# Kernel optimization log

Measured on AMD Instinct MI355X. Metric: run time of the kernel, lower is better.

Reference implementation:

```python
import jax, jax.numpy as jnp
import numpy as np
import math

B, S, D = 1, 2048, 2048
NQ, NKV = 32, 8
HD = D // NQ            # 64
NREP = NQ // NKV        # 4
EPS = 1e-6


def _rope_tables(seq_len, head_dim, theta=10000.0):
    half = head_dim // 2
    inv_freq = 1.0 / (theta ** (np.arange(0, half, dtype=np.float32) / half))
    t = np.arange(seq_len, dtype=np.float32)
    freqs = np.outer(t, inv_freq)  # [S, half]
    return jnp.asarray(np.cos(freqs)), jnp.asarray(np.sin(freqs))


def _rmsnorm(x, g, eps=EPS):
    denom = jnp.sqrt(jnp.mean(x * x, axis=-1, keepdims=True) + eps)
    return x / denom * g


def _rope(x, cos, sin):
    # x: [B, S, H, HD]; cos/sin: [S, HD//2]
    half = x.shape[-1] // 2
    x1, x2 = x[..., :half], x[..., half:]
    c = cos[None, :, None, :]
    s = sin[None, :, None, :]
    return jnp.concatenate([x1 * c - x2 * s, x1 * s + x2 * c], axis=-1)


def setup_inputs() -> dict:
    key = jax.random.key(0)
    ks = jax.random.split(key, 6)
    scale = 1.0 / math.sqrt(D)
    x = jax.random.normal(ks[0], (B, S, D), dtype=jnp.float32)
    Wq = jax.random.normal(ks[1], (D, NQ * HD), dtype=jnp.float32) * scale
    Wk = jax.random.normal(ks[2], (D, NKV * HD), dtype=jnp.float32) * scale
    Wv = jax.random.normal(ks[3], (D, NKV * HD), dtype=jnp.float32) * scale
    Wo = jax.random.normal(ks[4], (NQ * HD, D), dtype=jnp.float32) * scale
    g_q = jnp.ones((HD,), dtype=jnp.float32)
    g_k = jnp.ones((HD,), dtype=jnp.float32)
    cos, sin = _rope_tables(S, HD)
    return {"x": x, "cos": cos, "sin": sin, "g_q": g_q, "g_k": g_k,
            "Wq": Wq, "Wk": Wk, "Wv": Wv, "Wo": Wo}


def reference(x, cos, sin, g_q, g_k, Wq, Wk, Wv, Wo):
    bs, seq, _ = x.shape
    Q = (x @ Wq).reshape(bs, seq, NQ, HD)
    K = (x @ Wk).reshape(bs, seq, NKV, HD)
    V = (x @ Wv).reshape(bs, seq, NKV, HD)
    Q = _rope(_rmsnorm(Q, g_q), cos, sin)
    K = _rope(_rmsnorm(K, g_k), cos, sin)
    # GQA: repeat_interleave KV heads to match Q heads
    K = jnp.repeat(K, NREP, axis=2)  # [B,S,NQ,HD]
    V = jnp.repeat(V, NREP, axis=2)
    # scores: [B, H, S, S]
    scores = jnp.einsum('bshd,bthd->bhst', Q, K) / math.sqrt(HD)
    mask = jnp.triu(jnp.ones((seq, seq), dtype=bool), k=1)
    scores = jnp.where(mask, -jnp.inf, scores)
    attn = jax.nn.softmax(scores, axis=-1)
    out = jnp.einsum('bhst,bthd->bshd', attn, V).reshape(bs, seq, NQ * HD)
    return out @ Wo
```

## Files before the change

### kernel.cpp

```cpp
#include <hip/hip_runtime.h>
#include <hip/hip_bf16.h>
#include <math.h>

#define S 2048
#define D 2048
#define NQ 32
#define NKV 8
#define HD 64
#define HALF 32
#define NREP 4
#define QKV_N 3072
#define KCOL 2048
#define VCOL 2560

typedef unsigned short ushort_t;
typedef __attribute__((ext_vector_type(8))) short bf16x8;
typedef __attribute__((ext_vector_type(4))) float f32x4;
typedef float f4 __attribute__((ext_vector_type(4)));

__device__ __forceinline__ ushort_t f2bf(float f) {
    __hip_bfloat16 h = __float2bfloat16(f);
    return *reinterpret_cast<ushort_t*>(&h);
}
__device__ __forceinline__ float bf2f(ushort_t u) {
    __hip_bfloat16 h = *reinterpret_cast<__hip_bfloat16*>(&u);
    return __bfloat162float(h);
}

__device__ __forceinline__ void load_lds16(const ushort_t* g, ushort_t* l) {
    __builtin_amdgcn_global_load_lds(
        (const __attribute__((address_space(1))) unsigned int*)g,
        (__attribute__((address_space(3))) unsigned int*)l,
        16, 0, 0);
}

__global__ __launch_bounds__(256) void prep_all(const float* __restrict__ x,
                                                ushort_t* __restrict__ Xb,
                                                const float* __restrict__ Wq,
                                                const float* __restrict__ Wk,
                                                const float* __restrict__ Wv,
                                                ushort_t* __restrict__ WqkvT) {
    __shared__ float tile[32][33];
    const int b = blockIdx.x;
    if (b < 4096) {
        int i = (b * 256 + threadIdx.x) * 4;
        f4 v = *(const f4*)&x[i];
        Xb[i + 0] = f2bf(v[0]);
        Xb[i + 1] = f2bf(v[1]);
        Xb[i + 2] = f2bf(v[2]);
        Xb[i + 3] = f2bf(v[3]);
        return;
    }
    const float* src; int N, row_off, t;
    if (b < 8192)      { src = Wq; N = 2048; row_off = 0;    t = b - 4096; }
    else if (b < 9216) { src = Wk; N = 512;  row_off = 2048; t = b - 8192; }
    else               { src = Wv; N = 512;  row_off = 2560; t = b - 9216; }
    const int ntn = N / 32;
    const int n0 = (t % ntn) * 32, k0 = (t / ntn) * 32;
    const int tx = threadIdx.x & 31, ty = threadIdx.x >> 5;
    #pragma unroll
    for (int i = 0; i < 32; i += 8)
        tile[ty + i][tx] = src[(size_t)(k0 + ty + i) * N + (n0 + tx)];
    __syncthreads();
    #pragma unroll
    for (int i = 0; i < 32; i += 8)
        WqkvT[(size_t)(row_off + n0 + ty + i) * 2048 + (k0 + tx)] = f2bf(tile[tx][ty + i]);
}

template <typename OutT>
__global__ __launch_bounds__(256) void gemm64(const ushort_t* __restrict__ A,
                                              const ushort_t* __restrict__ BT,
                                              OutT* __restrict__ C,
                                              int M, int N, int Kdim) {
    __shared__ ushort_t As[64][64];
    __shared__ ushort_t Bs[64][64];
    const int tid = threadIdx.x;
    const int w = tid >> 6, lane = tid & 63;
    const int r16 = lane & 15, quad = lane >> 4;
    const int wm = (w >> 1) * 32, wn = (w & 1) * 32;
    const int bm = blockIdx.y * 64, bn = blockIdx.x * 64;
    const int srow = lane >> 3;
    const int jl = (lane & 7) ^ srow;
    const int rx = r16 & 7;

    f32x4 acc[2][2];
    #pragma unroll
    for (int r = 0; r < 2; ++r)
        #pragma unroll
        for (int c = 0; c < 2; ++c) acc[r][c] = (f32x4){0.f, 0.f, 0.f, 0.f};

    for (int k0 = 0; k0 < Kdim; k0 += 64) {
        __syncthreads();
        #pragma unroll
        for (int i = 0; i < 2; ++i) {
            int rbase = w * 16 + i * 8;
            load_lds16(A  + (size_t)(bm + rbase + srow) * Kdim + k0 + jl * 8, &As[rbase][0]);
            load_lds16(BT + (size_t)(bn + rbase + srow) * Kdim + k0 + jl * 8, &Bs[rbase][0]);
        }
        __syncthreads();

        #pragma unroll
        for (int h = 0; h < 2; ++h) {
            bf16x8 af[2], bfr[2];
            #pragma unroll
            for (int r = 0; r < 2; ++r)
                af[r]  = *(const bf16x8*)&As[wm + 16 * r + r16][((quad + 4 * h) ^ rx) * 8];
            #pragma unroll
            for (int c = 0; c < 2; ++c)
                bfr[c] = *(const bf16x8*)&Bs[wn + 16 * c + r16][((quad + 4 * h) ^ rx) * 8];
            #pragma unroll
            for (int r = 0; r < 2; ++r)
                #pragma unroll
                for (int c = 0; c < 2; ++c)
                    acc[r][c] = __builtin_amdgcn_mfma_f32_16x16x32_bf16(af[r], bfr[c], acc[r][c], 0, 0, 0);
        }
    }

    #pragma unroll
    for (int r = 0; r < 2; ++r)
        #pragma unroll
        for (int c = 0; c < 2; ++c)
            #pragma unroll
            for (int reg = 0; reg < 4; ++reg) {
                int row = bm + wm + 16 * r + quad * 4 + reg;
                int col = bn + wn + 16 * c + r16;
                float v = acc[r][c][reg];
                if constexpr (sizeof(OutT) == 2) C[(size_t)row * N + col] = (OutT)f2bf(v);
                else                             C[(size_t)row * N + col] = (OutT)v;
            }
}

__global__ __launch_bounds__(256) void rms_rope_vwo(ushort_t* __restrict__ QKV,
                                                    const float* __restrict__ gq,
                                                    const float* __restrict__ gk,
                                                    const float* __restrict__ cosT,
                                                    const float* __restrict__ sinT,
                                                    ushort_t* __restrict__ VTg,
                                                    const float* __restrict__ Wo,
                                                    ushort_t* __restrict__ WoT) {
    const int y = blockIdx.y, xb = blockIdx.x;
    if (y < 10) {
        const int s = xb;
        const int w = threadIdx.x >> 6;
        const int hh = y * 4 + w;
        const int d = threadIdx.x & 63;
        const float* g;
        int col;
        if (hh < NQ) { g = gq; col = hh * HD; }
        else         { g = gk; col = KCOL + (hh - NQ) * HD; }
        ushort_t* xp = QKV + (size_t)s * QKV_N + col;
        float v = bf2f(xp[d]);
        float ss = v * v;
        #pragma unroll
        for (int off = 32; off > 0; off >>= 1) ss += __shfl_down(ss, off);
        ss = __shfl(ss, 0);
        float inv = rsqrtf(ss * (1.0f / HD) + 1e-6f);
        float xn = v * inv * g[d];
        float other = __shfl(xn, d ^ 32);
        float c = cosT[(size_t)s * HALF + (d & 31)];
        float sn = sinT[(size_t)s * HALF + (d & 31)];
        float outv = (d < HALF) ? (xn * c - other * sn) : (other * sn + xn * c);
        xp[d] = f2bf(outv);
        return;
    }
    const int tx = threadIdx.x & 31, ty = threadIdx.x >> 5;
    if (y == 10 && xb < 1024) {
        __shared__ ushort_t vt[32][33];
        const int s0 = (xb & 63) * 32, d0 = (xb >> 6) * 32;
        #pragma unroll
        for (int i = 0; i < 32; i += 8)
            vt[ty + i][tx] = QKV[(size_t)(s0 + ty + i) * QKV_N + VCOL + d0 + tx];
        __syncthreads();
        #pragma unroll
        for (int i = 0; i < 32; i += 8)
            VTg[(size_t)(d0 + ty + i) * S + s0 + tx] = vt[tx][ty + i];
        return;
    }
    int idx;
    if (y == 10)      idx = xb - 1024;
    else if (y == 11) idx = 1024 + xb;
    else              idx = 3072 + xb;
    if (idx < 0 || idx >= 4096) return;
    __shared__ float wt[32][33];
    const int n0 = (idx & 63) * 32, k0 = (idx >> 6) * 32;
    #pragma unroll
    for (int i = 0; i < 32; i += 8)
        wt[ty + i][tx] = Wo[(size_t)(k0 + ty + i) * 2048 + (n0 + tx)];
    __syncthreads();
    #pragma unroll
    for (int i = 0; i < 32; i += 8)
        WoT[(size_t)(n0 + ty + i) * 2048 + (k0 + tx)] = f2bf(wt[tx][ty + i]);
}

__global__ __launch_bounds__(256) void zero_acc(f4* __restrict__ AccBuf4,
                                                f4* __restrict__ AccL4) {
    int i = blockIdx.x * 256 + threadIdx.x;
    if (i < 524288) AccBuf4[i] = (f4){0.f, 0.f, 0.f, 0.f};
    else if (i < 532480) AccL4[i - 524288] = (f4){0.f, 0.f, 0.f, 0.f};
}

__global__ __launch_bounds__(256) void flash_attn_mfma(const ushort_t* __restrict__ QKV,
                                                       const ushort_t* __restrict__ VTg,
                                                       ushort_t* __restrict__ O,
                                                       float* __restrict__ AccBuf,
                                                       float* __restrict__ AccL) {
    __shared__ ushort_t Ks[2][32][64];
    __shared__ ushort_t Vt[2][64][32];
    __shared__ ushort_t Ps[4][16][40];

    const int bx = blockIdx.x;
    int qt, tb, te;
    bool atom;
    if (bx < 16) { qt = 16 + bx; tb = 0; te = 32; atom = true; }
    else         { qt = 47 - bx; atom = (qt >= 16); tb = atom ? 32 : 0; te = 2 * qt + 2; }

    const int q0 = qt * 64;
    const int h  = blockIdx.y;
    const int kvh = h >> 2;
    const int tid = threadIdx.x;
    const int w = tid >> 6, lane = tid & 63;
    const int r16 = lane & 15, quad = lane >> 4;
    const int kcol = KCOL + kvh * HD;
    const int vtrow0 = kvh * HD;
    const int krow = lane >> 3;
    const int jl = (lane & 7) ^ krow;
    const int vrow = lane >> 2;
    const int jv = (lane & 3) ^ (vrow & 3);
    const int rx = r16 & 7;
    const int rx3 = r16 & 3;

    const ushort_t* qrow = QKV + (size_t)(q0 + 16 * w + r16) * QKV_N + h * HD;
    bf16x8 qf0, qf1;
    {
        bf16x8 r0 = *(const bf16x8*)(qrow + quad * 8);
        bf16x8 r1 = *(const bf16x8*)(qrow + quad * 8 + 32);
        #pragma unroll
        for (int j = 0; j < 8; ++j) {
            qf0[j] = (short)f2bf(bf2f((ushort_t)r0[j]) * 0.18033688f);
            qf1[j] = (short)f2bf(bf2f((ushort_t)r1[j]) * 0.18033688f);
        }
    }

    bf16x8 onesf;
    {
        ushort_t ov = (r16 == 0) ? (ushort_t)0x3F80 : (ushort_t)0;
        #pragma unroll
        for (int j = 0; j < 8; ++j) onesf[j] = (short)ov;
    }

    f32x4 accO[4];
    f32x4 accL = (f32x4){0.f, 0.f, 0.f, 0.f};
    #pragma unroll
    for (int c = 0; c < 4; ++c) accO[c] = (f32x4){0.f, 0.f, 0.f, 0.f};

    auto stage = [&](int b, int t) {
        const int kb = t * 32;
        load_lds16(QKV + (size_t)(kb + w * 8 + krow) * QKV_N + kcol + jl * 8,
                   &Ks[b][w * 8][0]);
        load_lds16(VTg + (size_t)(vtrow0 + w * 16 + vrow) * S + kb + jv * 8,
                   &Vt[b][w * 16][0]);
    };

    stage(tb & 1, tb);

    for (int t = tb; t < te; ++t) {
        __syncthreads();
        if (t + 1 < te) stage((t + 1) & 1, t + 1);

        const ushort_t (*K_)[64] = Ks[t & 1];
        const ushort_t (*V_)[32] = Vt[t & 1];
        const int rel = t * 32 - q0;
        const bool maskt = (rel >= 0);

        f32x4 sc[2];
        #pragma unroll
        for (int c = 0; c < 2; ++c) {
            bf16x8 kf0 = *(const bf16x8*)&K_[16 * c + r16][(quad ^ rx) * 8];
            bf16x8 kf1 = *(const bf16x8*)&K_[16 * c + r16][((quad + 4) ^ rx) * 8];
            f32x4 z = (f32x4){0.f, 0.f, 0.f, 0.f};
            z = __builtin_amdgcn_mfma_f32_16x16x32_bf16(qf0, kf0, z, 0, 0, 0);
            z = __builtin_amdgcn_mfma_f32_16x16x32_bf16(qf1, kf1, z, 0, 0, 0);
            sc[c] = z;
        }

        #pragma unroll
        for (int c = 0; c < 2; ++c)
            #pragma unroll
            for (int reg = 0; reg < 4; ++reg) {
                float v = sc[c][reg];
                if (maskt && (rel + 16 * c + r16 > 16 * w + quad * 4 + reg)) v = -INFINITY;
                Ps[w][quad * 4 + reg][16 * c + r16] = f2bf(exp2f(v));
            }

        bf16x8 pf = *(const bf16x8*)&Ps[w][r16][quad * 8];

        accL = __builtin_amdgcn_mfma_f32_16x16x32_bf16(pf, onesf, accL, 0, 0, 0);
        #pragma unroll
        for (int c = 0; c < 4; ++c) {
            bf16x8 vf = *(const bf16x8*)&V_[16 * c + r16][(quad ^ rx3) * 8];
            accO[c] = __builtin_amdgcn_mfma_f32_16x16x32_bf16(pf, vf, accO[c], 0, 0, 0);
        }
    }

    if (!atom) {
        #pragma unroll
        for (int reg = 0; reg < 4; ++reg) {
            float l = __shfl(accL[reg], lane & 48);
            float invl = 1.0f / l;
            int row = q0 + 16 * w + quad * 4 + reg;
            ushort_t* op = O + (size_t)row * D + h * HD;
            #pragma unroll
            for (int c = 0; c < 4; ++c)
                op[16 * c + r16] = f2bf(accO[c][reg] * invl);
        }
    } else {
        const int pair = (qt - 16) * 32 + h;
        float* ab = AccBuf + (size_t)pair * 4096;
        #pragma unroll
        for (int reg = 0; reg < 4; ++reg) {
            int row = 16 * w + quad * 4 + reg;
            #pragma unroll
            for (int c = 0; c < 4; ++c)
                atomicAdd(&ab[row * 64 + 16 * c + r16], accO[c][reg]);
        }
        if (r16 == 0) {
            #pragma unroll
            for (int reg = 0; reg < 4; ++reg)
                atomicAdd(&AccL[pair * 64 + 16 * w + quad * 4 + reg], accL[reg]);
        }
    }
}

__global__ __launch_bounds__(256) void normalize_o(const float* __restrict__ AccBuf,
                                                   const float* __restrict__ AccL,
                                                   ushort_t* __restrict__ O) {
    const int pair = blockIdx.x;
    const int qt = 16 + (pair >> 5);
    const int h  = pair & 31;
    const float* ab = AccBuf + (size_t)pair * 4096;
    const float* lp = AccL + pair * 64;
    for (int i = threadIdx.x; i < 4096; i += 256) {
        int row = i >> 6, d = i & 63;
        O[(size_t)(qt * 64 + row) * D + h * HD + d] = f2bf(ab[i] / lp[row]);
    }
}

extern "C" void kernel_launch(void* const* d_in, const int* in_sizes, int n_in,
                              void* d_out, int out_size, void* d_ws, size_t ws_size,
                              hipStream_t stream) {
    const float* x    = (const float*)d_in[0];
    const float* cosT = (const float*)d_in[1];
    const float* sinT = (const float*)d_in[2];
    const float* g_q  = (const float*)d_in[3];
    const float* g_k  = (const float*)d_in[4];
    const float* Wq   = (const float*)d_in[5];
    const float* Wk   = (const float*)d_in[6];
    const float* Wv   = (const float*)d_in[7];
    const float* Wo   = (const float*)d_in[8];
    float* out = (float*)d_out;

    char* base = (char*)d_ws;
    ushort_t* Xb    = (ushort_t*)base;
    ushort_t* WqkvT = (ushort_t*)(base + 8388608);
    ushort_t* QKVb  = (ushort_t*)(base + 20971520);
    ushort_t* WoT   = (ushort_t*)(base + 8388608);
    ushort_t* VTg   = (ushort_t*)(base + 16777216);
    float*    AccL  = (float*)(base + 18874368);
    float*    AccBuf = (float*)d_out;
    ushort_t* Ob    = Xb;

    prep_all<<<10240, 256, 0, stream>>>(x, Xb, Wq, Wk, Wv, WqkvT);
    gemm64<ushort_t><<<dim3(QKV_N / 64, S / 64), 256, 0, stream>>>(Xb, WqkvT, QKVb, S, QKV_N, D);
    rms_rope_vwo<<<dim3(2048, 13), 256, 0, stream>>>(QKVb, g_q, g_k, cosT, sinT, VTg, Wo, WoT);
    zero_acc<<<2080, 256, 0, stream>>>((f4*)AccBuf, (f4*)AccL);
    flash_attn_mfma<<<dim3(48, NQ), 256, 0, stream>>>(QKVb, VTg, Ob, AccBuf, AccL);
    normalize_o<<<512, 256, 0, stream>>>(AccBuf, AccL, Ob);
    gemm64<float><<<dim3(D / 64, S / 64), 256, 0, stream>>>(Ob, WoT, out, S, D, D);
}
```

Before: 257.5 us.

## Fuse RMSNorm/RoPE and V transpose into QKV GEMM epilogue, widen attention KV tiles

Adds a dedicated QKV GEMM whose epilogue applies RMSNorm and RoPE per head and writes V already transposed, which removes the separate rms_rope_vwo pass and its extra read and write of QKV. The accumulator zeroing moves into prep_all and the Wo transpose moves into the normalize kernel, cutting two launches. Flash attention now processes 64-key tiles instead of 32, halving loop iterations and barriers at the cost of more LDS. Workspace buffers are relocated into the output region.

```diff
diff --git a/kernel.cpp b/kernel.cpp
--- a/kernel.cpp
+++ b/kernel.cpp
@@ -16,6 +16,7 @@
 typedef unsigned short ushort_t;
 typedef __attribute__((ext_vector_type(8))) short bf16x8;
 typedef __attribute__((ext_vector_type(4))) float f32x4;
+typedef __attribute__((ext_vector_type(4))) unsigned short us4;
 typedef float f4 __attribute__((ext_vector_type(4)));
 
 __device__ __forceinline__ ushort_t f2bf(float f) {
@@ -39,7 +40,9 @@
                                                 const float* __restrict__ Wq,
                                                 const float* __restrict__ Wk,
                                                 const float* __restrict__ Wv,
-                                                ushort_t* __restrict__ WqkvT) {
+                                                ushort_t* __restrict__ WqkvT,
+                                                f4* __restrict__ AccBuf4,
+                                                f4* __restrict__ AccL4) {
     __shared__ float tile[32][33];
     const int b = blockIdx.x;
     if (b < 4096) {
@@ -51,6 +54,16 @@
         Xb[i + 3] = f2bf(v[3]);
         return;
     }
+    if (b >= 10240) {
+        if (b < 12288) {
+            int i = (b - 10240) * 256 + threadIdx.x;
+            AccBuf4[i] = (f4){0.f, 0.f, 0.f, 0.f};
+        } else {
+            int i = (b - 12288) * 256 + threadIdx.x;
+            if (i < 8192) AccL4[i] = (f4){0.f, 0.f, 0.f, 0.f};
+        }
+        return;
+    }
     const float* src; int N, row_off, t;
     if (b < 8192)      { src = Wq; N = 2048; row_off = 0;    t = b - 4096; }
     else if (b < 9216) { src = Wk; N = 512;  row_off = 2048; t = b - 8192; }
@@ -65,6 +78,117 @@
     #pragma unroll
     for (int i = 0; i < 32; i += 8)
         WqkvT[(size_t)(row_off + n0 + ty + i) * 2048 + (k0 + tx)] = f2bf(tile[tx][ty + i]);
+}
+
+__global__ __launch_bounds__(256) void gemm_qkv(const ushort_t* __restrict__ A,
+                                                const ushort_t* __restrict__ BT,
+                                                ushort_t* __restrict__ QKVb,
+                                                ushort_t* __restrict__ VTg,
+                                                const float* __restrict__ gq,
+                                                const float* __restrict__ gk,
+                                                const float* __restrict__ cosT,
+                                                const float* __restrict__ sinT) {
+    __shared__ ushort_t SM[8448];
+    ushort_t (*As)[32] = (ushort_t(*)[32])SM;
+    ushort_t (*Bs)[32] = (ushort_t(*)[32])(SM + 4096);
+    ushort_t (*Epi)[66] = (ushort_t(*)[66])SM;
+
+    const int tid = threadIdx.x;
+    const int w = tid >> 6, lane = tid & 63;
+    const int r16 = lane & 15, quad = lane >> 4;
+    const int wm = (w >> 1) * 64, wn = (w & 1) * 32;
+    const int bm = blockIdx.y * 128;
+    const int hcol = blockIdx.x;
+    const int bn = hcol * 64;
+    const int sr = lane >> 2;
+    const int sc8 = (lane & 3) * 8;
+
+    f32x4 acc[4][2];
+    #pragma unroll
+    for (int r = 0; r < 4; ++r)
+        #pragma unroll
+        for (int c = 0; c < 2; ++c) acc[r][c] = (f32x4){0.f, 0.f, 0.f, 0.f};
+
+    for (int k0 = 0; k0 < 2048; k0 += 32) {
+        __syncthreads();
+        #pragma unroll
+        for (int i = 0; i < 2; ++i) {
+            int rowt = w * 32 + i * 16;
+            load_lds16(A + (size_t)(bm + rowt + sr) * 2048 + k0 + sc8, &As[rowt][0]);
+        }
+        load_lds16(BT + (size_t)(bn + w * 16 + sr) * 2048 + k0 + sc8, &Bs[w * 16][0]);
+        __syncthreads();
+
+        bf16x8 af[4], bfr[2];
+        #pragma unroll
+        for (int r = 0; r < 4; ++r) af[r]  = *(const bf16x8*)&As[wm + 16 * r + r16][quad * 8];
+        #pragma unroll
+        for (int c = 0; c < 2; ++c) bfr[c] = *(const bf16x8*)&Bs[wn + 16 * c + r16][quad * 8];
+        #pragma unroll
+        for (int r = 0; r < 4; ++r)
+            #pragma unroll
+            for (int c = 0; c < 2; ++c)
+                acc[r][c] = __builtin_amdgcn_mfma_f32_16x16x32_bf16(af[r], bfr[c], acc[r][c], 0, 0, 0);
+    }
+
+    if (hcol >= 40) {
+        const int vd0 = (hcol - 40) * 64;
+        #pragma unroll
+        for (int r = 0; r < 4; ++r)
+            #pragma unroll
+            for (int c = 0; c < 2; ++c) {
+                int col = wn + 16 * c + r16;
+                int row0 = wm + 16 * r + quad * 4;
+                us4 pk;
+                #pragma unroll
+                for (int reg = 0; reg < 4; ++reg) pk[reg] = f2bf(acc[r][c][reg]);
+                *(us4*)&VTg[(size_t)(vd0 + col) * S + bm + row0] = pk;
+            }
+        return;
+    }
+
+    __syncthreads();
+    #pragma unroll
+    for (int r = 0; r < 4; ++r)
+        #pragma unroll
+        for (int c = 0; c < 2; ++c)
+            #pragma unroll
+            for (int reg = 0; reg < 4; ++reg)
+                Epi[wm + 16 * r + quad * 4 + reg][wn + 16 * c + r16] = f2bf(acc[r][c][reg]);
+    __syncthreads();
+
+    const float* g = (hcol < 32) ? gq : gk;
+    const int colbase = (hcol < 32) ? hcol * 64 : KCOL + (hcol - 32) * 64;
+    const int row = tid >> 1;
+    const int half = tid & 1;
+    const int cbase = half * 32;
+    const int s_glob = bm + row;
+
+    float xv[32], pv[32];
+    float ss = 0.f;
+    #pragma unroll
+    for (int j = 0; j < 32; ++j) {
+        xv[j] = bf2f(Epi[row][cbase + j]);
+        pv[j] = bf2f(Epi[row][(cbase ^ 32) + j]);
+        ss += xv[j] * xv[j];
+    }
+    ss += __shfl_xor(ss, 1);
+    float inv = rsqrtf(ss * (1.0f / HD) + 1e-6f);
+
+    ushort_t outp[32];
+    #pragma unroll
+    for (int j = 0; j < 32; ++j) {
+        float xn = xv[j] * inv * g[cbase + j];
+        float xp = pv[j] * inv * g[(cbase ^ 32) + j];
+        float cs = cosT[(size_t)s_glob * HALF + j];
+        float sn = sinT[(size_t)s_glob * HALF + j];
+        float o = half ? (xp * sn + xn * cs) : (xn * cs - xp * sn);
+        outp[j] = f2bf(o);
+    }
+    ushort_t* dst = QKVb + (size_t)s_glob * QKV_N + colbase + cbase;
+    #pragma unroll
+    for (int j = 0; j < 32; j += 8)
+        *(bf16x8*)&dst[j] = *(const bf16x8*)&outp[j];
 }
 
 template <typename OutT>
@@ -130,89 +254,20 @@
             }
 }
 
-__global__ __launch_bounds__(256) void rms_rope_vwo(ushort_t* __restrict__ QKV,
-                                                    const float* __restrict__ gq,
-                                                    const float* __restrict__ gk,
-                                                    const float* __restrict__ cosT,
-                                                    const float* __restrict__ sinT,
-                                                    ushort_t* __restrict__ VTg,
-                                                    const float* __restrict__ Wo,
-                                                    ushort_t* __restrict__ WoT) {
-    const int y = blockIdx.y, xb = blockIdx.x;
-    if (y < 10) {
-        const int s = xb;
-        const int w = threadIdx.x >> 6;
-        const int hh = y * 4 + w;
-        const int d = threadIdx.x & 63;
-        const float* g;
-        int col;
-        if (hh < NQ) { g = gq; col = hh * HD; }
-        else         { g = gk; col = KCOL + (hh - NQ) * HD; }
-        ushort_t* xp = QKV + (size_t)s * QKV_N + col;
-        float v = bf2f(xp[d]);
-        float ss = v * v;
-        #pragma unroll
-        for (int off = 32; off > 0; off >>= 1) ss += __shfl_down(ss, off);
-        ss = __shfl(ss, 0);
-        float inv = rsqrtf(ss * (1.0f / HD) + 1e-6f);
-        float xn = v * inv * g[d];
-        float other = __shfl(xn, d ^ 32);
-        float c = cosT[(size_t)s * HALF + (d & 31)];
-        float sn = sinT[(size_t)s * HALF + (d & 31)];
-        float outv = (d < HALF) ? (xn * c - other * sn) : (other * sn + xn * c);
-        xp[d] = f2bf(outv);
-        return;
-    }
-    const int tx = threadIdx.x & 31, ty = threadIdx.x >> 5;
-    if (y == 10 && xb < 1024) {
-        __shared__ ushort_t vt[32][33];
-        const int s0 = (xb & 63) * 32, d0 = (xb >> 6) * 32;
-        #pragma unroll
-        for (int i = 0; i < 32; i += 8)
-            vt[ty + i][tx] = QKV[(size_t)(s0 + ty + i) * QKV_N + VCOL + d0 + tx];
-        __syncthreads();
-        #pragma unroll
-        for (int i = 0; i < 32; i += 8)
-            VTg[(size_t)(d0 + ty + i) * S + s0 + tx] = vt[tx][ty + i];
-        return;
-    }
-    int idx;
-    if (y == 10)      idx = xb - 1024;
-    else if (y == 11) idx = 1024 + xb;
-    else              idx = 3072 + xb;
-    if (idx < 0 || idx >= 4096) return;
-    __shared__ float wt[32][33];
-    const int n0 = (idx & 63) * 32, k0 = (idx >> 6) * 32;
-    #pragma unroll
-    for (int i = 0; i < 32; i += 8)
-        wt[ty + i][tx] = Wo[(size_t)(k0 + ty + i) * 2048 + (n0 + tx)];
-    __syncthreads();
-    #pragma unroll
-    for (int i = 0; i < 32; i += 8)
-        WoT[(size_t)(n0 + ty + i) * 2048 + (k0 + tx)] = f2bf(wt[tx][ty + i]);
-}
-
-__global__ __launch_bounds__(256) void zero_acc(f4* __restrict__ AccBuf4,
-                                                f4* __restrict__ AccL4) {
-    int i = blockIdx.x * 256 + threadIdx.x;
-    if (i < 524288) AccBuf4[i] = (f4){0.f, 0.f, 0.f, 0.f};
-    else if (i < 532480) AccL4[i - 524288] = (f4){0.f, 0.f, 0.f, 0.f};
-}
-
 __global__ __launch_bounds__(256) void flash_attn_mfma(const ushort_t* __restrict__ QKV,
                                                        const ushort_t* __restrict__ VTg,
                                                        ushort_t* __restrict__ O,
                                                        float* __restrict__ AccBuf,
                                                        float* __restrict__ AccL) {
-    __shared__ ushort_t Ks[2][32][64];
-    __shared__ ushort_t Vt[2][64][32];
-    __shared__ ushort_t Ps[4][16][40];
+    __shared__ ushort_t Ks[2][64][64];
+    __shared__ ushort_t Vt[2][64][64];
+    __shared__ ushort_t Ps[4][16][72];
 
     const int bx = blockIdx.x;
     int qt, tb, te;
     bool atom;
-    if (bx < 16) { qt = 16 + bx; tb = 0; te = 32; atom = true; }
-    else         { qt = 47 - bx; atom = (qt >= 16); tb = atom ? 32 : 0; te = 2 * qt + 2; }
+    if (bx < 16) { qt = 16 + bx; tb = 0; te = 16; atom = true; }
+    else         { qt = 47 - bx; atom = (qt >= 16); tb = atom ? 16 : 0; te = qt + 1; }
 
     const int q0 = qt * 64;
     const int h  = blockIdx.y;
@@ -222,12 +277,9 @@
     const int r16 = lane & 15, quad = lane >> 4;
     const int kcol = KCOL + kvh * HD;
     const int vtrow0 = kvh * HD;
-    const int krow = lane >> 3;
-    const int jl = (lane & 7) ^ krow;
-    const int vrow = lane >> 2;
-    const int jv = (lane & 3) ^ (vrow & 3);
+    const int rsub = lane >> 3;
+    const int jlog = (lane & 7) ^ rsub;
     const int rx = r16 & 7;
-    const int rx3 = r16 & 3;
 
     const ushort_t* qrow = QKV + (size_t)(q0 + 16 * w + r16) * QKV_N + h * HD;
     bf16x8 qf0, qf1;
@@ -253,28 +305,29 @@
     #pragma unroll
     for (int c = 0; c < 4; ++c) accO[c] = (f32x4){0.f, 0.f, 0.f, 0.f};
 
-    auto stage = [&](int b, int t) {
-        const int kb = t * 32;
-        load_lds16(QKV + (size_t)(kb + w * 8 + krow) * QKV_N + kcol + jl * 8,
-                   &Ks[b][w * 8][0]);
-        load_lds16(VTg + (size_t)(vtrow0 + w * 16 + vrow) * S + kb + jv * 8,
-                   &Vt[b][w * 16][0]);
+    auto stage = [&](int b, int t0) {
+        #pragma unroll
+        for (int i = 0; i < 2; ++i) {
+            int base = w * 16 + i * 8;
+            int row = base + rsub;
+            load_lds16(QKV + (size_t)(t0 + row) * QKV_N + kcol + jlog * 8, &Ks[b][base][0]);
+            load_lds16(VTg + (size_t)(vtrow0 + row) * S + t0 + jlog * 8, &Vt[b][base][0]);
+        }
     };
 
-    stage(tb & 1, tb);
+    stage(tb & 1, tb * 64);
 
     for (int t = tb; t < te; ++t) {
         __syncthreads();
-        if (t + 1 < te) stage((t + 1) & 1, t + 1);
+        if (t + 1 < te) stage((t + 1) & 1, (t + 1) * 64);
 
         const ushort_t (*K_)[64] = Ks[t & 1];
-        const ushort_t (*V_)[32] = Vt[t & 1];
-        const int rel = t * 32 - q0;
-        const bool maskt = (rel >= 0);
-
-        f32x4 sc[2];
-        #pragma unroll
-        for (int c = 0; c < 2; ++c) {
+        const ushort_t (*V_)[64] = Vt[t & 1];
+        const bool diag = (t == qt);
+
+        f32x4 sc[4];
+        #pragma unroll
+        for (int c = 0; c < 4; ++c) {
             bf16x8 kf0 = *(const bf16x8*)&K_[16 * c + r16][(quad ^ rx) * 8];
             bf16x8 kf1 = *(const bf16x8*)&K_[16 * c + r16][((quad + 4) ^ rx) * 8];
             f32x4 z = (f32x4){0.f, 0.f, 0.f, 0.f};
@@ -284,21 +337,26 @@
         }
 
         #pragma unroll
-        for (int c = 0; c < 2; ++c)
+        for (int c = 0; c < 4; ++c)
             #pragma unroll
             for (int reg = 0; reg < 4; ++reg) {
                 float v = sc[c][reg];
-                if (maskt && (rel + 16 * c + r16 > 16 * w + quad * 4 + reg)) v = -INFINITY;
+                if (diag && (16 * c + r16 > 16 * w + quad * 4 + reg)) v = -INFINITY;
                 Ps[w][quad * 4 + reg][16 * c + r16] = f2bf(exp2f(v));
             }
 
-        bf16x8 pf = *(const bf16x8*)&Ps[w][r16][quad * 8];
-
-        accL = __builtin_amdgcn_mfma_f32_16x16x32_bf16(pf, onesf, accL, 0, 0, 0);
+        bf16x8 pf0 = *(const bf16x8*)&Ps[w][r16][quad * 8];
+        bf16x8 pf1 = *(const bf16x8*)&Ps[w][r16][quad * 8 + 32];
+
+        accL = __builtin_amdgcn_mfma_f32_16x16x32_bf16(pf0, onesf, accL, 0, 0, 0);
+        accL = __builtin_amdgcn_mfma_f32_16x16x32_bf16(pf1, onesf, accL, 0, 0, 0);
+
         #pragma unroll
         for (int c = 0; c < 4; ++c) {
-            bf16x8 vf = *(const bf16x8*)&V_[16 * c + r16][(quad ^ rx3) * 8];
-            accO[c] = __builtin_amdgcn_mfma_f32_16x16x32_bf16(pf, vf, accO[c], 0, 0, 0);
+            bf16x8 vf0 = *(const bf16x8*)&V_[16 * c + r16][(quad ^ rx) * 8];
+            bf16x8 vf1 = *(const bf16x8*)&V_[16 * c + r16][((quad + 4) ^ rx) * 8];
+            accO[c] = __builtin_amdgcn_mfma_f32_16x16x32_bf16(pf0, vf0, accO[c], 0, 0, 0);
+            accO[c] = __builtin_amdgcn_mfma_f32_16x16x32_bf16(pf1, vf1, accO[c], 0, 0, 0);
         }
     }
 
@@ -331,18 +389,34 @@
     }
 }
 
-__global__ __launch_bounds__(256) void normalize_o(const float* __restrict__ AccBuf,
-                                                   const float* __restrict__ AccL,
-                                                   ushort_t* __restrict__ O) {
-    const int pair = blockIdx.x;
-    const int qt = 16 + (pair >> 5);
-    const int h  = pair & 31;
-    const float* ab = AccBuf + (size_t)pair * 4096;
-    const float* lp = AccL + pair * 64;
-    for (int i = threadIdx.x; i < 4096; i += 256) {
-        int row = i >> 6, d = i & 63;
-        O[(size_t)(qt * 64 + row) * D + h * HD + d] = f2bf(ab[i] / lp[row]);
-    }
+__global__ __launch_bounds__(256) void normalize_wo(const float* __restrict__ AccBuf,
+                                                    const float* __restrict__ AccL,
+                                                    ushort_t* __restrict__ O,
+                                                    const float* __restrict__ Wo,
+                                                    ushort_t* __restrict__ WoT) {
+    const int b = blockIdx.x;
+    if (b < 512) {
+        const int qt = 16 + (b >> 5);
+        const int h  = b & 31;
+        const float* ab = AccBuf + (size_t)b * 4096;
+        const float* lp = AccL + b * 64;
+        for (int i = threadIdx.x; i < 4096; i += 256) {
+            int row = i >> 6, d = i & 63;
+            O[(size_t)(qt * 64 + row) * D + h * HD + d] = f2bf(ab[i] / lp[row]);
+        }
+        return;
+    }
+    __shared__ float wt[32][33];
+    const int idx = b - 512;
+    const int n0 = (idx & 63) * 32, k0 = (idx >> 6) * 32;
+    const int tx = threadIdx.x & 31, ty = threadIdx.x >> 5;
+    #pragma unroll
+    for (int i = 0; i < 32; i += 8)
+        wt[ty + i][tx] = Wo[(size_t)(k0 + ty + i) * 2048 + (n0 + tx)];
+    __syncthreads();
+    #pragma unroll
+    for (int i = 0; i < 32; i += 8)
+        WoT[(size_t)(n0 + ty + i) * 2048 + (k0 + tx)] = f2bf(wt[tx][ty + i]);
 }
 
 extern "C" void kernel_launch(void* const* d_in, const int* in_sizes, int n_in,
@@ -360,20 +434,19 @@
     float* out = (float*)d_out;
 
     char* base = (char*)d_ws;
-    ushort_t* Xb    = (ushort_t*)base;
-    ushort_t* WqkvT = (ushort_t*)(base + 8388608);
-    ushort_t* QKVb  = (ushort_t*)(base + 20971520);
-    ushort_t* WoT   = (ushort_t*)(base + 8388608);
-    ushort_t* VTg   = (ushort_t*)(base + 16777216);
-    float*    AccL  = (float*)(base + 18874368);
-    float*    AccBuf = (float*)d_out;
-    ushort_t* Ob    = Xb;
-
-    prep_all<<<10240, 256, 0, stream>>>(x, Xb, Wq, Wk, Wv, WqkvT);
-    gemm64<ushort_t><<<dim3(QKV_N / 64, S / 64), 256, 0, stream>>>(Xb, WqkvT, QKVb, S, QKV_N, D);
-    rms_rope_vwo<<<dim3(2048, 13), 256, 0, stream>>>(QKVb, g_q, g_k, cosT, sinT, VTg, Wo, WoT);
-    zero_acc<<<2080, 256, 0, stream>>>((f4*)AccBuf, (f4*)AccL);
+    char* ob   = (char*)d_out;
+    ushort_t* Xb     = (ushort_t*)base;
+    ushort_t* WqkvT  = (ushort_t*)(base + 8388608);
+    ushort_t* QKVb   = (ushort_t*)(base + 20971520);
+    ushort_t* WoT    = (ushort_t*)(base + 8388608);
+    ushort_t* Ob     = Xb;
+    float*    AccBuf = (float*)ob;
+    ushort_t* VTg    = (ushort_t*)(ob + 8388608);
+    float*    AccL   = (float*)(ob + 10485760);
+
+    prep_all<<<12320, 256, 0, stream>>>(x, Xb, Wq, Wk, Wv, WqkvT, (f4*)AccBuf, (f4*)AccL);
+    gemm_qkv<<<dim3(48, 16), 256, 0, stream>>>(Xb, WqkvT, QKVb, VTg, g_q, g_k, cosT, sinT);
     flash_attn_mfma<<<dim3(48, NQ), 256, 0, stream>>>(QKVb, VTg, Ob, AccBuf, AccL);
-    normalize_o<<<512, 256, 0, stream>>>(AccBuf, AccL, Ob);
+    normalize_wo<<<4608, 256, 0, stream>>>(AccBuf, AccL, Ob, Wo, WoT);
     gemm64<float><<<dim3(D / 64, S / 64), 256, 0, stream>>>(Ob, WoT, out, S, D, D);
 }
```

Result: slower. 270.8 us (+5.2%).
